# Performance work log

Measured on AMD Instinct MI355X. Metric: run time of the kernel, lower is better.

The kernel has to match this reference:

```python
import jax, jax.numpy as jnp
import numpy as np

EPS = 1e-5
SLOPE = 0.2


def setup_inputs() -> dict:
    key = jax.random.key(0)
    ks = jax.random.split(key, 8)
    B, D, N = 8, 60, 1024
    dims = [(64, 120), (64, 64), (128, 64), (256, 128), (256, 512), (1024, 256)]
    inp = {"x": jax.random.normal(ks[0], (B, D, N), dtype=jnp.float32)}
    for i, (o, c) in enumerate(dims, 1):
        inp[f"w{i}"] = jax.random.normal(ks[i], (o, c), dtype=jnp.float32) / np.sqrt(c).astype(np.float32)
        inp[f"b{i}"] = jnp.zeros((o,), jnp.float32)
        inp[f"g{i}"] = jnp.ones((o,), jnp.float32)
        inp[f"be{i}"] = jnp.zeros((o,), jnp.float32)
    inp["k"] = 20
    return inp


def knn_idx(x, k):
    # x: [B, D, N] -> idx [B, N, k] of nearest neighbors (negative sq dist topk)
    inner = -2.0 * jnp.einsum('bdn,bdm->bnm', x, x)
    xx = jnp.sum(x * x, axis=1)  # [B, N]
    pd = -xx[:, :, None] - inner - xx[:, None, :]
    _, idx = jax.lax.top_k(pd, k)
    return idx


def get_graph_feature(x, k):
    # x: [B, D, N] -> [B, 2D, N, k]
    B, D, N = x.shape
    idx = knn_idx(x, k)  # [B, N, k]
    xt = jnp.transpose(x, (0, 2, 1))  # [B, N, D]
    nbr = xt[jnp.arange(B)[:, None, None], idx]  # [B, N, k, D]
    ctr = xt[:, :, None, :]  # [B, N, 1, D]
    feat = jnp.concatenate([nbr - ctr, jnp.broadcast_to(ctr, nbr.shape)], axis=-1)
    return jnp.transpose(feat, (0, 3, 1, 2))  # [B, 2D, N, k]


def lrelu(x):
    return jnp.where(x >= 0, x, SLOPE * x)


def bn(x, g, b, axes):
    # training-mode batch norm (biased variance), channel axis = 1
    m = jnp.mean(x, axis=axes, keepdims=True)
    v = jnp.mean((x - m) ** 2, axis=axes, keepdims=True)
    sh = [1] * x.ndim
    sh[1] = -1
    return (x - m) * jax.lax.rsqrt(v + EPS) * g.reshape(sh) + b.reshape(sh)


def conv2d1x1(x, w, b):
    return jnp.einsum('bcnk,oc->bonk', x, w) + b[None, :, None, None]


def conv1d1x1(x, w, b):
    return jnp.einsum('bcn,oc->bon', x, w) + b[None, :, None]


def reference(x, w1, b1, g1, be1, w2, b2, g2, be2, w3, b3, g3, be3,
              w4, b4, g4, be4, w5, b5, g5, be5, w6, b6, g6, be6, k):
    h = get_graph_feature(x, k)                             # [B,120,N,k]
    h = lrelu(bn(conv2d1x1(h, w1, b1), g1, be1, (0, 2, 3)))
    x1 = jnp.max(h, axis=-1)
    h = lrelu(bn(conv2d1x1(h, w2, b2), g2, be2, (0, 2, 3)))
    x2 = jnp.max(h, axis=-1)
    h = lrelu(bn(conv2d1x1(h, w3, b3), g3, be3, (0, 2, 3)))
    x3 = jnp.max(h, axis=-1)
    h = lrelu(bn(conv2d1x1(h, w4, b4), g4, be4, (0, 2, 3)))
    x4 = jnp.max(h, axis=-1)
    h = jnp.concatenate([x1, x2, x3, x4], axis=1)           # [B,512,N]
    h = lrelu(bn(conv1d1x1(h, w5, b5), g5, be5, (0, 2)))
    h = lrelu(bn(conv1d1x1(h, w6, b6), g6, be6, (0, 2)))
    return jnp.transpose(h, (0, 2, 1))                      # [B,N,emb_dims]
```

## Files before the change

kernel.cpp:

```cpp
#include <hip/hip_runtime.h>
#include <hip/hip_bf16.h>
#include <math.h>

#define B_ 8
#define D_ 60
#define N_ 1024
#define K_ 20
#define P1_ 8192
#define P2_ 163840

typedef __attribute__((ext_vector_type(8))) short bf16x8;
typedef __attribute__((ext_vector_type(4))) short bf16x4;
typedef __attribute__((ext_vector_type(4))) float f32x4;

__device__ inline float b2f(short s) { return __uint_as_float(((unsigned)(unsigned short)s) << 16); }
__device__ inline short f2b(float f) { __hip_bfloat16 h = __float2bfloat16(f); return *(short*)&h; }

#define OFF_IDX   0ull
#define OFF_XX    655360ull
#define OFF_STATS 688128ull
#define OFF_XT    720896ull
#define OFF_WB    1769472ull
#define OFF_XC    2662400ull
#define OFF_H5    11051008ull
#define OFF_H6    15245312ull
#define OFF_BIGA  32022528ull
#define OFF_H1    73965568ull
#define OFF_H2    94937088ull
#define OFF_H4    115908608ull
#define OFF_PART  199794688ull
#define OFF_PART2 202444800ull

#define WO1 0
#define WO2 8192
#define WO3 12288
#define WO4 20480
#define WO5 53248
#define WO6 184320

#define SO1 0
#define SO2 64
#define SO3 128
#define SO4 256
#define SO5 512
#define SO6 768
#define NCH_TOT 1792

__global__ __launch_bounds__(256) void k_xx(const float* __restrict__ x,
                                            float* __restrict__ xx) {
  int bn = blockIdx.x * 256 + threadIdx.x;
  int b = bn >> 10, n = bn & 1023;
  const float* xb = x + (size_t)b * D_ * N_ + n;
  float s = 0.f;
  for (int d = 0; d < D_; ++d) { float v = xb[(size_t)d * N_]; s += v * v; }
  xx[bn] = s;
}

__global__ __launch_bounds__(256) void k_pd(const float* __restrict__ x,
                                            const float* __restrict__ xx,
                                            float* __restrict__ pd) {
  __shared__ float lnn[D_][64];
  __shared__ float lmm[D_][128];
  int tid = threadIdx.x;
  int m0 = blockIdx.x * 128, n0 = blockIdx.y * 64, b = blockIdx.z;
  const float* xb = x + (size_t)b * D_ * N_;
  #pragma unroll
  for (int i = 0; i < 15; ++i) {
    int idx = tid + i * 256;
    int d = idx >> 6, col = idx & 63;
    lnn[d][col] = xb[(size_t)d * N_ + n0 + col];
  }
  #pragma unroll
  for (int i = 0; i < 30; ++i) {
    int idx = tid + i * 256;
    int d = idx >> 7, col = idx & 127;
    lmm[d][col] = xb[(size_t)d * N_ + m0 + col];
  }
  __syncthreads();
  int tn = tid >> 5, tm = tid & 31;
  float acc[8][4];
  #pragma unroll
  for (int i = 0; i < 8; ++i)
    #pragma unroll
    for (int j = 0; j < 4; ++j) acc[i][j] = 0.f;
  for (int d = 0; d < D_; ++d) {
    f32x4 mv  = *(const f32x4*)&lmm[d][tm * 4];
    f32x4 nva = *(const f32x4*)&lnn[d][tn * 8];
    f32x4 nvb = *(const f32x4*)&lnn[d][tn * 8 + 4];
    #pragma unroll
    for (int i = 0; i < 4; ++i)
      #pragma unroll
      for (int j = 0; j < 4; ++j) {
        acc[i][j]     = fmaf(nva[i], mv[j], acc[i][j]);
        acc[4 + i][j] = fmaf(nvb[i], mv[j], acc[4 + i][j]);
      }
  }
  const float* xxb = xx + b * 1024;
  f32x4 xxm = *(const f32x4*)(xxb + m0 + tm * 4);
  #pragma unroll
  for (int i = 0; i < 8; ++i) {
    int n = n0 + tn * 8 + i;
    float xxn = xxb[n];
    f32x4 o;
    #pragma unroll
    for (int j = 0; j < 4; ++j) o[j] = 2.f * acc[i][j] - xxn - xxm[j];
    *(f32x4*)(pd + ((size_t)(b * 1024 + n) * 1024) + m0 + tm * 4) = o;
  }
}

__global__ __launch_bounds__(256) void k_sel(const float* __restrict__ pd,
                                             int* __restrict__ idxb) {
  int tid = threadIdx.x;
  int wave = tid >> 6, lane = tid & 63;
  int bn = blockIdx.x * 4 + wave;
  const float* row = pd + (size_t)bn * 1024;
  int mbase = lane * 16;
  f32x4 r0 = *(const f32x4*)(row + mbase);
  f32x4 r1 = *(const f32x4*)(row + mbase + 4);
  f32x4 r2 = *(const f32x4*)(row + mbase + 8);
  f32x4 r3 = *(const f32x4*)(row + mbase + 12);
  float v[16];
  #pragma unroll
  for (int j = 0; j < 4; ++j) { v[j] = r0[j]; v[4 + j] = r1[j]; v[8 + j] = r2[j]; v[12 + j] = r3[j]; }
  int* outp = idxb + (size_t)bn * K_;
  for (int kk = 0; kk < K_; ++kk) {
    float bv = v[0]; int bj = 0;
    #pragma unroll
    for (int j = 1; j < 16; ++j)
      if (v[j] > bv) { bv = v[j]; bj = j; }
    int bi = mbase + bj;
    #pragma unroll
    for (int off = 1; off < 64; off <<= 1) {
      float ov = __shfl_xor(bv, off);
      int   oi = __shfl_xor(bi, off);
      if (ov > bv || (ov == bv && oi < bi)) { bv = ov; bi = oi; }
    }
    if (lane == 0) outp[kk] = bi;
    #pragma unroll
    for (int j = 0; j < 16; ++j)
      if (bi == mbase + j) v[j] = -INFINITY;
  }
}

__global__ __launch_bounds__(256) void k_xt(const float* __restrict__ x,
                                            short* __restrict__ xt) {
  int bn = blockIdx.x * 256 + threadIdx.x;
  int b = bn >> 10, n = bn & 1023;
  const float* xb = x + (size_t)b * D_ * N_ + n;
  short* row = xt + (size_t)bn * 64;
  for (int c = 0; c < 60; ++c) row[c] = f2b(xb[(size_t)c * N_]);
  row[60] = 0; row[61] = 0; row[62] = 0; row[63] = 0;
}

__global__ __launch_bounds__(256) void k_w1pad(const float* __restrict__ w1,
                                               short* __restrict__ wb) {
  int t = blockIdx.x * 256 + threadIdx.x;
  int o = t >> 7, c = t & 127;
  float v = 0.f;
  if (c < 60) v = w1[o * 120 + c];
  else if (c >= 64 && c < 124) v = w1[o * 120 + 60 + (c - 64)];
  wb[t] = f2b(v);
}

__global__ __launch_bounds__(256) void k_wcvt(const float* __restrict__ w2,
                                              const float* __restrict__ w3,
                                              const float* __restrict__ w4,
                                              const float* __restrict__ w5,
                                              const float* __restrict__ w6,
                                              short* __restrict__ wbase) {
  int t = blockIdx.x * 256 + threadIdx.x;
  if (t < 4096) wbase[WO2 + t] = f2b(w2[t]);
  else if (t < 12288) wbase[WO3 + (t - 4096)] = f2b(w3[t - 4096]);
  else if (t < 45056) wbase[WO4 + (t - 12288)] = f2b(w4[t - 12288]);
  else if (t < 176128) wbase[WO5 + (t - 45056)] = f2b(w5[t - 45056]);
  else if (t < 438272) wbase[WO6 + (t - 176128)] = f2b(w6[t - 176128]);
}

__global__ __launch_bounds__(256) void k_feat(const short* __restrict__ xt,
                                              const int* __restrict__ idxb,
                                              short* __restrict__ feat) {
  int t = blockIdx.x * 256 + threadIdx.x;
  int p = t >> 4, chunk = t & 15;
  int bn = p / K_;
  int nbr = (bn & ~1023) + idxb[p];
  bf16x8 o;
  if (chunk < 8) {
    bf16x8 c8 = *(const bf16x8*)(xt + (size_t)bn * 64 + chunk * 8);
    bf16x8 n8 = *(const bf16x8*)(xt + (size_t)nbr * 64 + chunk * 8);
    #pragma unroll
    for (int r = 0; r < 8; ++r) o[r] = f2b(b2f(n8[r]) - b2f(c8[r]));
  } else {
    o = *(const bf16x8*)(xt + (size_t)bn * 64 + (chunk - 8) * 8);
  }
  *(bf16x8*)(feat + (size_t)p * 128 + chunk * 8) = o;
}

template <int K, int COUT, bool APPLY, bool STATS>
__global__ __launch_bounds__(256) void k_gemm(const short* __restrict__ in,
                                              const short* __restrict__ wb,
                                              const float* __restrict__ bias,
                                              const float* __restrict__ Ain,
                                              const float* __restrict__ Bin,
                                              float* __restrict__ part,
                                              short* __restrict__ out) {
  constexpr int PANEL = (K < 128) ? K : 128;
  constexpr int NPAN = K / PANEL;
  constexpr int CPR = PANEL / 8;
  constexpr int CSH = (CPR == 16) ? 4 : 3;
  constexpr int PK = PANEL + 8;
  constexpr int KS = PANEL / 32;
  __shared__ short ldsA[128 * PK];
  __shared__ short ldsW[64 * PK];
  __shared__ float ls[128];
  int tid = threadIdx.x;
  int w = tid >> 6, lane = tid & 63;
  int ln = lane & 15, quad = lane >> 4;
  int co0 = blockIdx.y * 64;
  const short* srcA = in + (size_t)blockIdx.x * 128 * K;
  const short* srcW = wb + (size_t)co0 * K;

  f32x4 acc[4][2];
  #pragma unroll
  for (int m = 0; m < 4; ++m)
    #pragma unroll
    for (int t = 0; t < 2; ++t) acc[m][t] = (f32x4){0.f, 0.f, 0.f, 0.f};

  for (int pan = 0; pan < NPAN; ++pan) {
    int kp = pan * PANEL;
    if (pan) __syncthreads();
    #pragma unroll
    for (int i = 0; i < CPR / 2; ++i) {
      int g = i * 256 + tid;
      int row = g >> CSH, c = g & (CPR - 1);
      bf16x8 v = *(const bf16x8*)(srcA + (size_t)row * K + kp + c * 8);
      if (APPLY) {
        f32x4 a0 = *(const f32x4*)(Ain + kp + c * 8);
        f32x4 a1 = *(const f32x4*)(Ain + kp + c * 8 + 4);
        f32x4 b0 = *(const f32x4*)(Bin + kp + c * 8);
        f32x4 b1 = *(const f32x4*)(Bin + kp + c * 8 + 4);
        #pragma unroll
        for (int j = 0; j < 8; ++j) {
          float aj = j < 4 ? a0[j] : a1[j - 4];
          float bj = j < 4 ? b0[j] : b1[j - 4];
          float f = b2f(v[j]) * aj + bj;
          f = f >= 0.f ? f : 0.2f * f;
          v[j] = f2b(f);
        }
      }
      *(bf16x8*)(ldsA + row * PK + c * 8) = v;
    }
    #pragma unroll
    for (int i = 0; i < CPR / 4; ++i) {
      int g = i * 256 + tid;
      int row = g >> CSH, c = g & (CPR - 1);
      *(bf16x8*)(ldsW + row * PK + c * 8) =
          *(const bf16x8*)(srcW + (size_t)row * K + kp + c * 8);
    }
    __syncthreads();
    #pragma unroll
    for (int ks = 0; ks < KS; ++ks) {
      bf16x8 a[4], bfr[2];
      #pragma unroll
      for (int m = 0; m < 4; ++m)
        a[m] = *(const bf16x8*)(ldsW + (m * 16 + ln) * PK + ks * 32 + quad * 8);
      #pragma unroll
      for (int t = 0; t < 2; ++t)
        bfr[t] = *(const bf16x8*)(ldsA + (w * 32 + t * 16 + ln) * PK + ks * 32 + quad * 8);
      #pragma unroll
      for (int m = 0; m < 4; ++m)
        #pragma unroll
        for (int t = 0; t < 2; ++t)
          acc[m][t] = __builtin_amdgcn_mfma_f32_16x16x32_bf16(a[m], bfr[t], acc[m][t], 0, 0, 0);
    }
  }
  #pragma unroll
  for (int m = 0; m < 4; ++m) {
    f32x4 bs = *(const f32x4*)(bias + co0 + m * 16 + quad * 4);
    #pragma unroll
    for (int t = 0; t < 2; ++t)
      #pragma unroll
      for (int r = 0; r < 4; ++r) acc[m][t][r] += bs[r];
  }
  #pragma unroll
  for (int m = 0; m < 4; ++m)
    #pragma unroll
    for (int t = 0; t < 2; ++t) {
      int p = blockIdx.x * 128 + w * 32 + t * 16 + ln;
      bf16x4 o;
      #pragma unroll
      for (int r = 0; r < 4; ++r) o[r] = f2b(acc[m][t][r]);
      *(bf16x4*)(out + (size_t)p * COUT + co0 + m * 16 + quad * 4) = o;
    }
  if (STATS) {
    __syncthreads();
    if (tid < 128) ls[tid] = 0.f;
    __syncthreads();
    #pragma unroll
    for (int m = 0; m < 4; ++m)
      #pragma unroll
      for (int r = 0; r < 4; ++r) {
        float v0 = acc[m][0][r], v1 = acc[m][1][r];
        float s = v0 + v1, ss = v0 * v0 + v1 * v1;
        #pragma unroll
        for (int off = 1; off < 16; off <<= 1) {
          s += __shfl_xor(s, off); ss += __shfl_xor(ss, off);
        }
        if (ln == 0) {
          atomicAdd(&ls[m * 16 + quad * 4 + r], s);
          atomicAdd(&ls[64 + m * 16 + quad * 4 + r], ss);
        }
      }
    __syncthreads();
    if (tid < 128)
      part[((size_t)blockIdx.y * gridDim.x + blockIdx.x) * 128 + tid] = ls[tid];
  }
}

__global__ __launch_bounds__(256) void k_red(const float* __restrict__ part, int NB,
                                             float* __restrict__ part2) {
  int cc = blockIdx.x, by = blockIdx.y;
  int tid = threadIdx.x;
  int rg = tid >> 5;
  int c4 = (tid & 31) * 4;
  int chunk = NB >> 5;
  const float* p = part + ((size_t)cc * NB + (size_t)by * chunk) * 128;
  f32x4 acc = (f32x4){0.f, 0.f, 0.f, 0.f};
  for (int r = rg; r < chunk; r += 8) {
    f32x4 v = *(const f32x4*)(p + (size_t)r * 128 + c4);
    acc[0] += v[0]; acc[1] += v[1]; acc[2] += v[2]; acc[3] += v[3];
  }
  __shared__ float lds[1024];
  *(f32x4*)(lds + tid * 4) = acc;
  __syncthreads();
  if (tid < 32) {
    f32x4 s = (f32x4){0.f, 0.f, 0.f, 0.f};
    #pragma unroll
    for (int g = 0; g < 8; ++g) {
      f32x4 v = *(const f32x4*)(lds + (g * 32 + tid) * 4);
      s[0] += v[0]; s[1] += v[1]; s[2] += v[2]; s[3] += v[3];
    }
    *(f32x4*)(part2 + ((size_t)cc * 32 + by) * 128 + tid * 4) = s;
  }
}

__global__ __launch_bounds__(256) void k_bnab(const float* __restrict__ part, int NB,
                                              const float* __restrict__ g,
                                              const float* __restrict__ be,
                                              float* __restrict__ A,
                                              float* __restrict__ Bp, float inv) {
  __shared__ float red[256];
  int tid = threadIdx.x;
  int j = tid & 127, h = tid >> 7;
  const float* p = part + (size_t)blockIdx.x * NB * 128;
  float s = 0.f;
  for (int bx = h; bx < NB; bx += 2) s += p[(size_t)bx * 128 + j];
  red[tid] = s;
  __syncthreads();
  if (tid < 128) red[tid] = red[tid] + red[tid + 128];
  __syncthreads();
  if (tid < 64) {
    int c = blockIdx.x * 64 + tid;
    float m = red[tid] * inv;
    float v = red[64 + tid] * inv - m * m;
    float a = g[c] * rsqrtf(v + 1e-5f);
    A[c] = a; Bp[c] = be[c] - m * a;
  }
}

template <int C>
__global__ __launch_bounds__(256) void k_apply_max(const short* __restrict__ h,
                                                   const float* __restrict__ A,
                                                   const float* __restrict__ Bp,
                                                   short* __restrict__ xcat, int xoff) {
  constexpr int CH = C / 4;
  int t = blockIdx.x * 256 + threadIdx.x;
  int bn = t / CH;
  int c0 = (t % CH) * 4;
  f32x4 a = *(const f32x4*)(A + c0);
  f32x4 b = *(const f32x4*)(Bp + c0);
  float m0 = -INFINITY, m1 = -INFINITY, m2 = -INFINITY, m3 = -INFINITY;
  size_t base = (size_t)bn * K_ * C + c0;
  for (int j = 0; j < K_; ++j) {
    bf16x4 v = *(const bf16x4*)(h + base + (size_t)j * C);
    float f0 = b2f(v[0]) * a[0] + b[0]; f0 = f0 >= 0.f ? f0 : 0.2f * f0;
    float f1 = b2f(v[1]) * a[1] + b[1]; f1 = f1 >= 0.f ? f1 : 0.2f * f1;
    float f2 = b2f(v[2]) * a[2] + b[2]; f2 = f2 >= 0.f ? f2 : 0.2f * f2;
    float f3 = b2f(v[3]) * a[3] + b[3]; f3 = f3 >= 0.f ? f3 : 0.2f * f3;
    m0 = fmaxf(m0, f0); m1 = fmaxf(m1, f1); m2 = fmaxf(m2, f2); m3 = fmaxf(m3, f3);
  }
  bf16x4 o;
  o[0] = f2b(m0); o[1] = f2b(m1); o[2] = f2b(m2); o[3] = f2b(m3);
  *(bf16x4*)(xcat + (size_t)bn * 512 + xoff + c0) = o;
}

__global__ __launch_bounds__(256) void k_apply_out(const short* __restrict__ h,
                                                   const float* __restrict__ A,
                                                   const float* __restrict__ Bp,
                                                   float* __restrict__ out) {
  int t = blockIdx.x * 256 + threadIdx.x;
  int c0 = (t & 255) * 4;
  f32x4 a = *(const f32x4*)(A + c0);
  f32x4 b = *(const f32x4*)(Bp + c0);
  bf16x4 v = *(const bf16x4*)(h + (size_t)t * 4);
  f32x4 o;
  #pragma unroll
  for (int r = 0; r < 4; ++r) {
    float f = b2f(v[r]) * a[r] + b[r];
    o[r] = f >= 0.f ? f : 0.2f * f;
  }
  *(f32x4*)(out + (size_t)t * 4) = o;
}

extern "C" void kernel_launch(void* const* d_in, const int* in_sizes, int n_in,
                              void* d_out, int out_size, void* d_ws, size_t ws_size,
                              hipStream_t stream) {
  const float* x   = (const float*)d_in[0];
  const float* w1  = (const float*)d_in[1];
  const float* b1  = (const float*)d_in[2];
  const float* g1  = (const float*)d_in[3];
  const float* be1 = (const float*)d_in[4];
  const float* w2  = (const float*)d_in[5];
  const float* b2  = (const float*)d_in[6];
  const float* g2  = (const float*)d_in[7];
  const float* be2 = (const float*)d_in[8];
  const float* w3  = (const float*)d_in[9];
  const float* b3  = (const float*)d_in[10];
  const float* g3  = (const float*)d_in[11];
  const float* be3 = (const float*)d_in[12];
  const float* w4  = (const float*)d_in[13];
  const float* b4  = (const float*)d_in[14];
  const float* g4  = (const float*)d_in[15];
  const float* be4 = (const float*)d_in[16];
  const float* w5  = (const float*)d_in[17];
  const float* b5  = (const float*)d_in[18];
  const float* g5  = (const float*)d_in[19];
  const float* be5 = (const float*)d_in[20];
  const float* w6  = (const float*)d_in[21];
  const float* b6  = (const float*)d_in[22];
  const float* g6  = (const float*)d_in[23];
  const float* be6 = (const float*)d_in[24];
  float* out = (float*)d_out;
  char* ws = (char*)d_ws;

  int*   idxb = (int*)(ws + OFF_IDX);
  float* xx   = (float*)(ws + OFF_XX);
  float* Aall = (float*)(ws + OFF_STATS);
  float* Ball = Aall + NCH_TOT;
  short* xt   = (short*)(ws + OFF_XT);
  short* wbb  = (short*)(ws + OFF_WB);
  short* xcat = (short*)(ws + OFF_XC);
  short* h5   = (short*)(ws + OFF_H5);
  short* h6   = (short*)(ws + OFF_H6);
  short* feat = (short*)(ws + OFF_BIGA);
  short* h1   = (short*)(ws + OFF_H1);
  short* h2   = (short*)(ws + OFF_H2);
  short* h3   = (short*)(ws + OFF_BIGA);
  short* h4   = (short*)(ws + OFF_H4);
  float* pd    = (float*)(ws + OFF_H4);
  float* part  = (float*)(ws + OFF_PART);
  float* part2 = (float*)(ws + OFF_PART2);

  k_xx <<<P1_ / 256, 256, 0, stream>>>(x, xx);
  k_pd <<<dim3(8, 16, 8), 256, 0, stream>>>(x, xx, pd);
  k_sel<<<P1_ / 4, 256, 0, stream>>>(pd, idxb);
  k_xt <<<P1_ / 256, 256, 0, stream>>>(x, xt);
  k_w1pad<<<32, 256, 0, stream>>>(w1, wbb + WO1);
  k_wcvt<<<1712, 256, 0, stream>>>(w2, w3, w4, w5, w6, wbb);
  k_feat<<<P2_ * 16 / 256, 256, 0, stream>>>(xt, idxb, feat);

  k_gemm<128, 64, false, true><<<dim3(P2_ / 128, 1), 256, 0, stream>>>(
      feat, wbb + WO1, b1, nullptr, nullptr, part, h1);
  k_red <<<dim3(1, 32), 256, 0, stream>>>(part, P2_ / 128, part2);
  k_bnab<<<1, 256, 0, stream>>>(part2, 32, g1, be1, Aall + SO1, Ball + SO1, 1.f / P2_);
  k_apply_max<64><<<P1_ * 16 / 256, 256, 0, stream>>>(h1, Aall + SO1, Ball + SO1, xcat, 0);

  k_gemm<64, 64, true, true><<<dim3(P2_ / 128, 1), 256, 0, stream>>>(
      h1, wbb + WO2, b2, Aall + SO1, Ball + SO1, part, h2);
  k_red <<<dim3(1, 32), 256, 0, stream>>>(part, P2_ / 128, part2);
  k_bnab<<<1, 256, 0, stream>>>(part2, 32, g2, be2, Aall + SO2, Ball + SO2, 1.f / P2_);
  k_apply_max<64><<<P1_ * 16 / 256, 256, 0, stream>>>(h2, Aall + SO2, Ball + SO2, xcat, 64);

  k_gemm<64, 128, true, true><<<dim3(P2_ / 128, 2), 256, 0, stream>>>(
      h2, wbb + WO3, b3, Aall + SO2, Ball + SO2, part, h3);
  k_red <<<dim3(2, 32), 256, 0, stream>>>(part, P2_ / 128, part2);
  k_bnab<<<2, 256, 0, stream>>>(part2, 32, g3, be3, Aall + SO3, Ball + SO3, 1.f / P2_);
  k_apply_max<128><<<P1_ * 32 / 256, 256, 0, stream>>>(h3, Aall + SO3, Ball + SO3, xcat, 128);

  k_gemm<128, 256, true, true><<<dim3(P2_ / 128, 4), 256, 0, stream>>>(
      h3, wbb + WO4, b4, Aall + SO3, Ball + SO3, part, h4);
  k_red <<<dim3(4, 32), 256, 0, stream>>>(part, P2_ / 128, part2);
  k_bnab<<<4, 256, 0, stream>>>(part2, 32, g4, be4, Aall + SO4, Ball + SO4, 1.f / P2_);
  k_apply_max<256><<<P1_ * 64 / 256, 256, 0, stream>>>(h4, Aall + SO4, Ball + SO4, xcat, 256);

  k_gemm<512, 256, false, true><<<dim3(P1_ / 128, 4), 256, 0, stream>>>(
      xcat, wbb + WO5, b5, nullptr, nullptr, part, h5);
  k_bnab<<<4, 256, 0, stream>>>(part, P1_ / 128, g5, be5, Aall + SO5, Ball + SO5, 1.f / P1_);

  k_gemm<256, 1024, true, true><<<dim3(P1_ / 128, 16), 256, 0, stream>>>(
      h5, wbb + WO6, b6, Aall + SO5, Ball + SO5, part, h6);
  k_bnab<<<16, 256, 0, stream>>>(part, P1_ / 128, g6, be6, Aall + SO6, Ball + SO6, 1.f / P1_);
  k_apply_out<<<P1_ * 256 / 256, 256, 0, stream>>>(h6, Aall + SO6, Ball + SO6, out);

  (void)in_sizes; (void)n_in; (void)out_size; (void)ws_size;
}
```

Measured before the change: 446.1 us.

## Fuse edge-feature gather into first GEMM and recompute layer-4 GEMM with fused BN/max

```diff
diff --git a/kernel.cpp b/kernel.cpp
--- a/kernel.cpp
+++ b/kernel.cpp
@@ -176,26 +176,7 @@
   else if (t < 438272) wbase[WO6 + (t - 176128)] = f2b(w6[t - 176128]);
 }
 
-__global__ __launch_bounds__(256) void k_feat(const short* __restrict__ xt,
-                                              const int* __restrict__ idxb,
-                                              short* __restrict__ feat) {
-  int t = blockIdx.x * 256 + threadIdx.x;
-  int p = t >> 4, chunk = t & 15;
-  int bn = p / K_;
-  int nbr = (bn & ~1023) + idxb[p];
-  bf16x8 o;
-  if (chunk < 8) {
-    bf16x8 c8 = *(const bf16x8*)(xt + (size_t)bn * 64 + chunk * 8);
-    bf16x8 n8 = *(const bf16x8*)(xt + (size_t)nbr * 64 + chunk * 8);
-    #pragma unroll
-    for (int r = 0; r < 8; ++r) o[r] = f2b(b2f(n8[r]) - b2f(c8[r]));
-  } else {
-    o = *(const bf16x8*)(xt + (size_t)bn * 64 + (chunk - 8) * 8);
-  }
-  *(bf16x8*)(feat + (size_t)p * 128 + chunk * 8) = o;
-}
-
-template <int K, int COUT, bool APPLY, bool STATS>
+template <int K, int COUT, bool APPLY, bool STATS, bool WRITE>
 __global__ __launch_bounds__(256) void k_gemm(const short* __restrict__ in,
                                               const short* __restrict__ wb,
                                               const float* __restrict__ bias,
@@ -281,16 +262,18 @@
       #pragma unroll
       for (int r = 0; r < 4; ++r) acc[m][t][r] += bs[r];
   }
-  #pragma unroll
-  for (int m = 0; m < 4; ++m)
-    #pragma unroll
-    for (int t = 0; t < 2; ++t) {
-      int p = blockIdx.x * 128 + w * 32 + t * 16 + ln;
-      bf16x4 o;
-      #pragma unroll
-      for (int r = 0; r < 4; ++r) o[r] = f2b(acc[m][t][r]);
-      *(bf16x4*)(out + (size_t)p * COUT + co0 + m * 16 + quad * 4) = o;
-    }
+  if (WRITE) {
+    #pragma unroll
+    for (int m = 0; m < 4; ++m)
+      #pragma unroll
+      for (int t = 0; t < 2; ++t) {
+        int p = blockIdx.x * 128 + w * 32 + t * 16 + ln;
+        bf16x4 o;
+        #pragma unroll
+        for (int r = 0; r < 4; ++r) o[r] = f2b(acc[m][t][r]);
+        *(bf16x4*)(out + (size_t)p * COUT + co0 + m * 16 + quad * 4) = o;
+      }
+  }
   if (STATS) {
     __syncthreads();
     if (tid < 128) ls[tid] = 0.f;
@@ -314,6 +297,218 @@
     if (tid < 128)
       part[((size_t)blockIdx.y * gridDim.x + blockIdx.x) * 128 + tid] = ls[tid];
   }
+}
+
+__global__ __launch_bounds__(256) void k_gemm1(const short* __restrict__ xt,
+                                               const int* __restrict__ idxb,
+                                               const short* __restrict__ wb,
+                                               const float* __restrict__ bias,
+                                               float* __restrict__ part,
+                                               short* __restrict__ out) {
+  constexpr int PK = 136, KS = 4;
+  __shared__ short ldsA[128 * PK];
+  __shared__ short ldsW[64 * PK];
+  __shared__ float ls[128];
+  int tid = threadIdx.x;
+  int w = tid >> 6, lane = tid & 63;
+  int ln = lane & 15, quad = lane >> 4;
+  int p0 = blockIdx.x * 128;
+  #pragma unroll
+  for (int i = 0; i < 8; ++i) {
+    int g = i * 256 + tid;
+    int row = g >> 4, c = g & 15;
+    int p = p0 + row;
+    int bn = p / K_;
+    int nbr = (bn & ~1023) + idxb[p];
+    bf16x8 v;
+    if (c < 8) {
+      bf16x8 cb = *(const bf16x8*)(xt + (size_t)bn * 64 + c * 8);
+      bf16x8 nb = *(const bf16x8*)(xt + (size_t)nbr * 64 + c * 8);
+      #pragma unroll
+      for (int j = 0; j < 8; ++j) v[j] = f2b(b2f(nb[j]) - b2f(cb[j]));
+    } else {
+      v = *(const bf16x8*)(xt + (size_t)bn * 64 + (c - 8) * 8);
+    }
+    *(bf16x8*)(ldsA + row * PK + c * 8) = v;
+  }
+  #pragma unroll
+  for (int i = 0; i < 4; ++i) {
+    int g = i * 256 + tid;
+    int row = g >> 4, c = g & 15;
+    *(bf16x8*)(ldsW + row * PK + c * 8) = *(const bf16x8*)(wb + (size_t)row * 128 + c * 8);
+  }
+  __syncthreads();
+  f32x4 acc[4][2];
+  #pragma unroll
+  for (int m = 0; m < 4; ++m)
+    #pragma unroll
+    for (int t = 0; t < 2; ++t) acc[m][t] = (f32x4){0.f, 0.f, 0.f, 0.f};
+  #pragma unroll
+  for (int ks = 0; ks < KS; ++ks) {
+    bf16x8 a[4], bfr[2];
+    #pragma unroll
+    for (int m = 0; m < 4; ++m)
+      a[m] = *(const bf16x8*)(ldsW + (m * 16 + ln) * PK + ks * 32 + quad * 8);
+    #pragma unroll
+    for (int t = 0; t < 2; ++t)
+      bfr[t] = *(const bf16x8*)(ldsA + (w * 32 + t * 16 + ln) * PK + ks * 32 + quad * 8);
+    #pragma unroll
+    for (int m = 0; m < 4; ++m)
+      #pragma unroll
+      for (int t = 0; t < 2; ++t)
+        acc[m][t] = __builtin_amdgcn_mfma_f32_16x16x32_bf16(a[m], bfr[t], acc[m][t], 0, 0, 0);
+  }
+  #pragma unroll
+  for (int m = 0; m < 4; ++m) {
+    f32x4 bs = *(const f32x4*)(bias + m * 16 + quad * 4);
+    #pragma unroll
+    for (int t = 0; t < 2; ++t) {
+      int p = p0 + w * 32 + t * 16 + ln;
+      bf16x4 o;
+      #pragma unroll
+      for (int r = 0; r < 4; ++r) { acc[m][t][r] += bs[r]; o[r] = f2b(acc[m][t][r]); }
+      *(bf16x4*)(out + (size_t)p * 64 + m * 16 + quad * 4) = o;
+    }
+  }
+  __syncthreads();
+  if (tid < 128) ls[tid] = 0.f;
+  __syncthreads();
+  #pragma unroll
+  for (int m = 0; m < 4; ++m)
+    #pragma unroll
+    for (int r = 0; r < 4; ++r) {
+      float v0 = acc[m][0][r], v1 = acc[m][1][r];
+      float s = v0 + v1, ss = v0 * v0 + v1 * v1;
+      #pragma unroll
+      for (int off = 1; off < 16; off <<= 1) {
+        s += __shfl_xor(s, off); ss += __shfl_xor(ss, off);
+      }
+      if (ln == 0) {
+        atomicAdd(&ls[m * 16 + quad * 4 + r], s);
+        atomicAdd(&ls[64 + m * 16 + quad * 4 + r], ss);
+      }
+    }
+  __syncthreads();
+  if (tid < 128)
+    part[(size_t)blockIdx.x * 128 + tid] = ls[tid];
+}
+
+__global__ __launch_bounds__(256) void k_gemm4b(const short* __restrict__ in,
+                                                const short* __restrict__ wb,
+                                                const float* __restrict__ bias,
+                                                const float* __restrict__ Ain,
+                                                const float* __restrict__ Bin,
+                                                const float* __restrict__ Aout,
+                                                const float* __restrict__ Bout,
+                                                unsigned* __restrict__ x4u) {
+  constexpr int PK = 136, KS = 4;
+  __shared__ short ldsA[128 * PK];
+  __shared__ short ldsW[64 * PK];
+  int tid = threadIdx.x;
+  int w = tid >> 6, lane = tid & 63;
+  int ln = lane & 15, quad = lane >> 4;
+  int co0 = blockIdx.y * 64;
+  int p0 = blockIdx.x * 128;
+  const short* srcA = in + (size_t)blockIdx.x * 128 * 128;
+  const short* srcW = wb + (size_t)co0 * 128;
+  #pragma unroll
+  for (int i = 0; i < 8; ++i) {
+    int g = i * 256 + tid;
+    int row = g >> 4, c = g & 15;
+    bf16x8 v = *(const bf16x8*)(srcA + (size_t)row * 128 + c * 8);
+    f32x4 a0 = *(const f32x4*)(Ain + c * 8);
+    f32x4 a1 = *(const f32x4*)(Ain + c * 8 + 4);
+    f32x4 b0 = *(const f32x4*)(Bin + c * 8);
+    f32x4 b1 = *(const f32x4*)(Bin + c * 8 + 4);
+    #pragma unroll
+    for (int j = 0; j < 8; ++j) {
+      float aj = j < 4 ? a0[j] : a1[j - 4];
+      float bj = j < 4 ? b0[j] : b1[j - 4];
+      float f = b2f(v[j]) * aj + bj;
+      f = f >= 0.f ? f : 0.2f * f;
+      v[j] = f2b(f);
+    }
+    *(bf16x8*)(ldsA + row * PK + c * 8) = v;
+  }
+  #pragma unroll
+  for (int i = 0; i < 4; ++i) {
+    int g = i * 256 + tid;
+    int row = g >> 4, c = g & 15;
+    *(bf16x8*)(ldsW + row * PK + c * 8) = *(const bf16x8*)(srcW + (size_t)row * 128 + c * 8);
+  }
+  __syncthreads();
+  f32x4 acc[4][2];
+  #pragma unroll
+  for (int m = 0; m < 4; ++m)
+    #pragma unroll
+    for (int t = 0; t < 2; ++t) acc[m][t] = (f32x4){0.f, 0.f, 0.f, 0.f};
+  #pragma unroll
+  for (int ks = 0; ks < KS; ++ks) {
+    bf16x8 a[4], bfr[2];
+    #pragma unroll
+    for (int m = 0; m < 4; ++m)
+      a[m] = *(const bf16x8*)(ldsW + (m * 16 + ln) * PK + ks * 32 + quad * 8);
+    #pragma unroll
+    for (int t = 0; t < 2; ++t)
+      bfr[t] = *(const bf16x8*)(ldsA + (w * 32 + t * 16 + ln) * PK + ks * 32 + quad * 8);
+    #pragma unroll
+    for (int m = 0; m < 4; ++m)
+      #pragma unroll
+      for (int t = 0; t < 2; ++t)
+        acc[m][t] = __builtin_amdgcn_mfma_f32_16x16x32_bf16(a[m], bfr[t], acc[m][t], 0, 0, 0);
+  }
+  #pragma unroll
+  for (int m = 0; m < 4; ++m) {
+    f32x4 bs = *(const f32x4*)(bias + co0 + m * 16 + quad * 4);
+    f32x4 ao = *(const f32x4*)(Aout + co0 + m * 16 + quad * 4);
+    f32x4 bo = *(const f32x4*)(Bout + co0 + m * 16 + quad * 4);
+    #pragma unroll
+    for (int t = 0; t < 2; ++t)
+      #pragma unroll
+      for (int r = 0; r < 4; ++r) {
+        float f = (acc[m][t][r] + bs[r]) * ao[r] + bo[r];
+        acc[m][t][r] = f >= 0.f ? f : 0.2f * f;
+      }
+  }
+  __syncthreads();
+  float* mt = (float*)ldsA;
+  #pragma unroll
+  for (int m = 0; m < 4; ++m)
+    #pragma unroll
+    for (int t = 0; t < 2; ++t)
+      #pragma unroll
+      for (int r = 0; r < 4; ++r)
+        mt[(m * 16 + quad * 4 + r) * 128 + w * 32 + t * 16 + ln] = acc[m][t][r];
+  __syncthreads();
+  int g0 = p0 / K_, g1 = (p0 + 127) / K_;
+  int ng = g1 - g0 + 1;
+  for (int tsk = tid; tsk < 64 * ng; tsk += 256) {
+    int col = tsk & 63, gi = tsk >> 6;
+    int gg = g0 + gi;
+    int ps = max(gg * K_, p0), pe = min(gg * K_ + K_, p0 + 128);
+    float mval = -INFINITY;
+    for (int q = ps; q < pe; ++q) mval = fmaxf(mval, mt[col * 128 + (q - p0)]);
+    unsigned u = __float_as_uint(mval);
+    u = (u & 0x80000000u) ? ~u : (u | 0x80000000u);
+    unsigned* dst = &x4u[(size_t)gg * 256 + co0 + col];
+    if (gg * K_ >= p0 && gg * K_ + K_ <= p0 + 128) *dst = u;
+    else atomicMax(dst, u);
+  }
+}
+
+__global__ __launch_bounds__(256) void k_cvt4(const unsigned* __restrict__ x4u,
+                                              short* __restrict__ xcat) {
+  int t = blockIdx.x * 256 + threadIdx.x;
+  int bn = t >> 6, c0 = (t & 63) * 4;
+  const unsigned* src = x4u + (size_t)bn * 256 + c0;
+  bf16x4 o;
+  #pragma unroll
+  for (int r = 0; r < 4; ++r) {
+    unsigned u = src[r];
+    u = (u & 0x80000000u) ? (u & 0x7FFFFFFFu) : ~u;
+    o[r] = f2b(__uint_as_float(u));
+  }
+  *(bf16x4*)(xcat + (size_t)bn * 512 + 256 + c0) = o;
 }
 
 __global__ __launch_bounds__(256) void k_red(const float* __restrict__ part, int NB,
@@ -451,12 +646,11 @@
   short* xcat = (short*)(ws + OFF_XC);
   short* h5   = (short*)(ws + OFF_H5);
   short* h6   = (short*)(ws + OFF_H6);
-  short* feat = (short*)(ws + OFF_BIGA);
   short* h1   = (short*)(ws + OFF_H1);
   short* h2   = (short*)(ws + OFF_H2);
   short* h3   = (short*)(ws + OFF_BIGA);
-  short* h4   = (short*)(ws + OFF_H4);
   float* pd    = (float*)(ws + OFF_H4);
+  unsigned* x4u = (unsigned*)(ws + OFF_H4);
   float* part  = (float*)(ws + OFF_PART);
   float* part2 = (float*)(ws + OFF_PART2);
 
@@ -466,37 +660,38 @@
   k_xt <<<P1_ / 256, 256, 0, stream>>>(x, xt);
   k_w1pad<<<32, 256, 0, stream>>>(w1, wbb + WO1);
   k_wcvt<<<1712, 256, 0, stream>>>(w2, w3, w4, w5, w6, wbb);
-  k_feat<<<P2_ * 16 / 256, 256, 0, stream>>>(xt, idxb, feat);
-
-  k_gemm<128, 64, false, true><<<dim3(P2_ / 128, 1), 256, 0, stream>>>(
-      feat, wbb + WO1, b1, nullptr, nullptr, part, h1);
+
+  k_gemm1<<<P2_ / 128, 256, 0, stream>>>(xt, idxb, wbb + WO1, b1, part, h1);
   k_red <<<dim3(1, 32), 256, 0, stream>>>(part, P2_ / 128, part2);
   k_bnab<<<1, 256, 0, stream>>>(part2, 32, g1, be1, Aall + SO1, Ball + SO1, 1.f / P2_);
   k_apply_max<64><<<P1_ * 16 / 256, 256, 0, stream>>>(h1, Aall + SO1, Ball + SO1, xcat, 0);
 
-  k_gemm<64, 64, true, true><<<dim3(P2_ / 128, 1), 256, 0, stream>>>(
+  k_gemm<64, 64, true, true, true><<<dim3(P2_ / 128, 1), 256, 0, stream>>>(
       h1, wbb + WO2, b2, Aall + SO1, Ball + SO1, part, h2);
   k_red <<<dim3(1, 32), 256, 0, stream>>>(part, P2_ / 128, part2);
   k_bnab<<<1, 256, 0, stream>>>(part2, 32, g2, be2, Aall + SO2, Ball + SO2, 1.f / P2_);
   k_apply_max<64><<<P1_ * 16 / 256, 256, 0, stream>>>(h2, Aall + SO2, Ball + SO2, xcat, 64);
 
-  k_gemm<64, 128, true, true><<<dim3(P2_ / 128, 2), 256, 0, stream>>>(
+  k_gemm<64, 128, true, true, true><<<dim3(P2_ / 128, 2), 256, 0, stream>>>(
       h2, wbb + WO3, b3, Aall + SO2, Ball + SO2, part, h3);
   k_red <<<dim3(2, 32), 256, 0, stream>>>(part, P2_ / 128, part2);
   k_bnab<<<2, 256, 0, stream>>>(part2, 32, g3, be3, Aall + SO3, Ball + SO3, 1.f / P2_);
   k_apply_max<128><<<P1_ * 32 / 256, 256, 0, stream>>>(h3, Aall + SO3, Ball + SO3, xcat, 128);
 
-  k_gemm<128, 256, true, true><<<dim3(P2_ / 128, 4), 256, 0, stream>>>(
-      h3, wbb + WO4, b4, Aall + SO3, Ball + SO3, part, h4);
+  k_gemm<128, 256, true, true, false><<<dim3(P2_ / 128, 4), 256, 0, stream>>>(
+      h3, wbb + WO4, b4, Aall + SO3, Ball + SO3, part, nullptr);
   k_red <<<dim3(4, 32), 256, 0, stream>>>(part, P2_ / 128, part2);
   k_bnab<<<4, 256, 0, stream>>>(part2, 32, g4, be4, Aall + SO4, Ball + SO4, 1.f / P2_);
-  k_apply_max<256><<<P1_ * 64 / 256, 256, 0, stream>>>(h4, Aall + SO4, Ball + SO4, xcat, 256);
-
-  k_gemm<512, 256, false, true><<<dim3(P1_ / 128, 4), 256, 0, stream>>>(
+  hipMemsetAsync(x4u, 0, (size_t)P1_ * 256 * 4, stream);
+  k_gemm4b<<<dim3(P2_ / 128, 4), 256, 0, stream>>>(
+      h3, wbb + WO4, b4, Aall + SO3, Ball + SO3, Aall + SO4, Ball + SO4, x4u);
+  k_cvt4<<<P1_ * 64 / 256, 256, 0, stream>>>(x4u, xcat);
+
+  k_gemm<512, 256, false, true, true><<<dim3(P1_ / 128, 4), 256, 0, stream>>>(
       xcat, wbb + WO5, b5, nullptr, nullptr, part, h5);
   k_bnab<<<4, 256, 0, stream>>>(part, P1_ / 128, g5, be5, Aall + SO5, Ball + SO5, 1.f / P1_);
 
-  k_gemm<256, 1024, true, true><<<dim3(P1_ / 128, 16), 256, 0, stream>>>(
+  k_gemm<256, 1024, true, true, true><<<dim3(P1_ / 128, 16), 256, 0, stream>>>(
       h5, wbb + WO6, b6, Aall + SO5, Ball + SO5, part, h6);
   k_bnab<<<16, 256, 0, stream>>>(part, P1_ / 128, g6, be6, Aall + SO6, Ball + SO6, 1.f / P1_);
   k_apply_out<<<P1_ * 256 / 256, 256, 0, stream>>>(h6, Aall + SO6, Ball + SO6, out);
```

Measured after the change: 490.4 us. 9.9% more time.
